# Optimization experiments

Measured on AMD Instinct MI355X. Metric: run time of the kernel, lower is better.

Reference implementation:

```python
import jax, jax.numpy as jnp
import numpy as np

N_HEADS = 8
TANH_CLIP = 10.0
NEG = -1e9  # finite stand-in for -inf so log_softmax/vjp stay NaN-free


def setup_inputs() -> dict:
    key = jax.random.key(0)
    ks = jax.random.split(key, 8)
    B, N, D = 256, 1000, 128
    embeddings = jax.random.normal(ks[0], (B, N, D), dtype=jnp.float32)
    W_node = jax.random.normal(ks[1], (D, 3 * D), dtype=jnp.float32) * (1.0 / np.sqrt(D))
    W_fixed = jax.random.normal(ks[2], (D, D), dtype=jnp.float32) * (1.0 / np.sqrt(D))
    W_step = jax.random.normal(ks[3], (2 * D, D), dtype=jnp.float32) * (1.0 / np.sqrt(2 * D))
    W_out = jax.random.normal(ks[4], (D, D), dtype=jnp.float32) * (1.0 / np.sqrt(D))
    first_idx = jax.random.randint(ks[5], (B,), 0, N)
    last_idx = jax.random.randint(ks[6], (B,), 0, N)
    mask = jax.random.randint(ks[7], (B, N), 0, 2).astype(jnp.bool_)
    mask = mask.at[:, 0].set(False)  # guarantee at least one feasible node
    return {"embeddings": embeddings, "W_node": W_node, "W_fixed": W_fixed,
            "W_step": W_step, "W_out": W_out, "first_idx": first_idx,
            "last_idx": last_idx, "mask": mask}


def reference(embeddings, W_node, W_fixed, W_step, W_out, first_idx, last_idx, mask):
    # One pointer-network decode step (TSP variant of AttentionModel._get_log_p),
    # including the _precompute projections.
    B, N, D = embeddings.shape
    H = N_HEADS
    dk = D // H

    # _precompute: fixed context + glimpse K/V + logit key
    graph_embed = embeddings.mean(axis=1)                       # [B, D]
    fixed_ctx = graph_embed @ W_fixed                           # [B, D]
    kvl = embeddings @ W_node                                   # [B, N, 3D]
    K, V, logit_K = jnp.split(kvl, 3, axis=-1)                  # each [B, N, D]

    # step context: cat(first-node emb, last-node emb) -> project to D
    b = jnp.arange(B)
    step_ctx = jnp.concatenate([embeddings[b, first_idx], embeddings[b, last_idx]], axis=-1)  # [B, 2D]
    q = fixed_ctx + step_ctx @ W_step                           # [B, D]

    # masked multi-head glimpse attention (q_len = 1)
    qh = q.reshape(B, H, dk)                                    # [B, H, dk]
    Kh = K.reshape(B, N, H, dk)
    Vh = V.reshape(B, N, H, dk)
    compat = jnp.einsum('bhd,bnhd->bhn', qh, Kh) / np.sqrt(dk)  # [B, H, N]
    compat = jnp.where(mask[:, None, :], NEG, compat)           # mask_inner
    attn = jax.nn.softmax(compat, axis=-1)
    heads = jnp.einsum('bhn,bnhd->bhd', attn, Vh)               # [B, H, dk]
    glimpse = heads.reshape(B, D) @ W_out                       # [B, D]

    # single-head logit attention with tanh clipping
    logits = jnp.einsum('bd,bnd->bn', glimpse, logit_K) / np.sqrt(D)  # [B, N]
    logits = jnp.tanh(logits) * TANH_CLIP
    logits = jnp.where(mask, NEG, logits)                       # mask_logits
    return jax.nn.log_softmax(logits, axis=-1)                  # [B, N]
```

## Files before the change

### kernel.cpp

```cpp
#include <hip/hip_runtime.h>


#define NEG (-1e9f)

__global__ void k_detect(const uint4* __restrict__ mw, int* __restrict__ flag)
{
    __shared__ int any_s;
    if (threadIdx.x == 0) any_s = 0;
    __syncthreads();
    unsigned acc = 0;
    #pragma unroll
    for (int i = 0; i < 4; ++i) {
        const uint4 v = mw[i * 256 + threadIdx.x];
        acc |= (v.x | v.y | v.z | v.w) & 0xFFFFFF00u;
    }
    if (acc) atomicOr(&any_s, 1);
    __syncthreads();
    if (threadIdx.x == 0) *flag = any_s;
}

__global__ __launch_bounds__(1024) void k_pre(
    const float* __restrict__ E, const float* __restrict__ Wn,
    const float* __restrict__ Wf, const float* __restrict__ Ws,
    const int* __restrict__ fi, const int* __restrict__ li,
    float* __restrict__ qkp)
{
    const int b = blockIdx.x;
    const int t = threadIdx.x;
    __shared__ float4 red4[1024];
    __shared__ float mu[128], e1[128], e2[128], q[128];
    __shared__ float qred[8][128];

    const float4* E4 = (const float4*)(E + (size_t)b * 128000);

    {
        const int c4 = t & 31, s = t >> 5;
        float4 acc = make_float4(0.f, 0.f, 0.f, 0.f);
        for (int r = s; r < 1000; r += 32) {
            float4 v = E4[r * 32 + c4];
            acc.x += v.x; acc.y += v.y; acc.z += v.z; acc.w += v.w;
        }
        red4[t] = acc;
    }
    if (t >= 512 && t < 544) {
        ((float4*)e1)[t - 512] = E4[fi[b] * 32 + (t - 512)];
    } else if (t >= 544 && t < 576) {
        ((float4*)e2)[t - 544] = E4[li[b] * 32 + (t - 544)];
    }
    __syncthreads();
    if (t < 32) {
        float4 acc = red4[t];
        #pragma unroll
        for (int s = 1; s < 32; ++s) {
            float4 v = red4[s * 32 + t];
            acc.x += v.x; acc.y += v.y; acc.z += v.z; acc.w += v.w;
        }
        const float inv = 1.0f / 1000.0f;
        ((float4*)mu)[t] = make_float4(acc.x * inv, acc.y * inv, acc.z * inv, acc.w * inv);
    }
    __syncthreads();
    {
        const int part = t >> 7, d = t & 127;
        float acc = 0.f;
        const int k0 = part * 48;
        for (int k = k0; k < k0 + 48; ++k) {
            const float s = (k < 128) ? mu[k] : (k < 256 ? e1[k - 128] : e2[k - 256]);
            const float w = (k < 128) ? Wf[k * 128 + d] : Ws[(k - 128) * 128 + d];
            acc += s * w;
        }
        qred[part][d] = acc;
    }
    __syncthreads();
    if (t < 128) {
        float acc = 0.f;
        #pragma unroll
        for (int p = 0; p < 8; ++p) acc += qred[p][t];
        q[t] = acc;
    }
    __syncthreads();
    {
        const int j = t & 127, cg = t >> 7;
        const float qj = q[j];
        for (int c0 = 0; c0 < 128; c0 += 8) {
            const int c = c0 + cg;
            float v = Wn[c * 384 + j] * qj;
            v += __shfl_down(v, 8, 16);
            v += __shfl_down(v, 4, 16);
            v += __shfl_down(v, 2, 16);
            v += __shfl_down(v, 1, 16);
            if ((j & 15) == 0) qkp[b * 1024 + (j >> 4) * 128 + c] = v * 0.25f;
        }
    }
}

__global__ __launch_bounds__(256) void k_glimpse(
    const float* __restrict__ E, const float* __restrict__ Wn,
    const float* __restrict__ Wo,
    const int* __restrict__ maskI, const unsigned char* __restrict__ maskB,
    const int* __restrict__ flag,
    const float* __restrict__ qkp, float* __restrict__ glp)
{
    const int b = blockIdx.x;
    const int t = threadIdx.x;
    __shared__ float4 qk4[256];
    __shared__ float4 Et[2048];
    __shared__ float pc[64 * 33];
    __shared__ float ct[64 * 9];
    __shared__ float pt[64 * 8];
    __shared__ float mh[8], lh[8], al[8];
    __shared__ float EbarF[8 * 128];
    __shared__ float heads[128];
    __shared__ float gl[128];

    const float4* E4 = (const float4*)(E + (size_t)b * 128000);
    const bool useB = (*flag != 0);

    {
        const int h = t >> 5, g = t & 31;
        qk4[h * 32 + (g ^ (g >> 3))] = ((const float4*)(qkp + b * 1024))[t];
    }
    if (t < 8) { mh[t] = -3e38f; lh[t] = 0.f; }
    float4 eacc[8];
    #pragma unroll
    for (int h = 0; h < 8; ++h) eacc[h] = make_float4(0.f, 0.f, 0.f, 0.f);
    const int c4 = t & 31, sl = t >> 5;
    const int rr = t >> 2, qq = t & 3;
    __syncthreads();

    for (int tile = 0; tile < 16; ++tile) {
        const int r0 = tile * 64;
        {
            const int g = r0 + rr;
            float4 v[8];
            if (g < 1000) {
                #pragma unroll
                for (int i = 0; i < 8; ++i) v[i] = E4[g * 32 + qq * 8 + i];
            } else {
                #pragma unroll
                for (int i = 0; i < 8; ++i) v[i] = make_float4(0.f, 0.f, 0.f, 0.f);
            }
            float pch[8];
            #pragma unroll
            for (int h = 0; h < 8; ++h) pch[h] = 0.f;
            #pragma unroll
            for (int i = 0; i < 8; ++i) {
                const int grp = qq * 8 + i;
                Et[rr * 32 + (grp ^ (rr & 7))] = v[i];
                #pragma unroll
                for (int h = 0; h < 8; ++h) {
                    float4 w = qk4[h * 32 + (grp ^ qq)];
                    pch[h] += v[i].x * w.x + v[i].y * w.y + v[i].z * w.z + v[i].w * w.w;
                }
            }
            #pragma unroll
            for (int h = 0; h < 8; ++h) pc[rr * 33 + qq * 8 + h] = pch[h];
        }
        __syncthreads();
        #pragma unroll
        for (int k = 0; k < 2; ++k) {
            const int idx = t + k * 256;
            const int row = idx >> 3, h = idx & 7;
            float s = pc[row * 33 + h] + pc[row * 33 + 8 + h]
                    + pc[row * 33 + 16 + h] + pc[row * 33 + 24 + h];
            const int g = r0 + row;
            const bool m = (g >= 1000) ||
                (useB ? (maskB[b * 1000 + g] != 0) : (maskI[b * 1000 + g] != 0));
            ct[row * 9 + h] = m ? NEG : s;
        }
        __syncthreads();
        if (t < 8) {
            float mt = -3e38f;
            for (int r = 0; r < 64; ++r) mt = fmaxf(mt, ct[r * 9 + t]);
            const float mnew = fmaxf(mh[t], mt);
            al[t] = __expf(mh[t] - mnew);
            mh[t] = mnew;
        }
        __syncthreads();
        #pragma unroll
        for (int k = 0; k < 2; ++k) {
            const int idx = t + k * 256;
            const int row = idx >> 3, h = idx & 7;
            pt[row * 8 + h] = __expf(ct[row * 9 + h] - mh[h]);
        }
        __syncthreads();
        if (t < 8) {
            float s = 0.f;
            for (int r = 0; r < 64; ++r) s += pt[r * 8 + t];
            lh[t] = lh[t] * al[t] + s;
        }
        {
            #pragma unroll
            for (int h = 0; h < 8; ++h) {
                const float a = al[h];
                eacc[h].x *= a; eacc[h].y *= a; eacc[h].z *= a; eacc[h].w *= a;
            }
            #pragma unroll
            for (int j = 0; j < 8; ++j) {
                const int r = sl * 8 + j;
                const float4 ev = Et[r * 32 + (c4 ^ (r & 7))];
                const float4 p0 = ((float4*)pt)[r * 2];
                const float4 p1 = ((float4*)pt)[r * 2 + 1];
                eacc[0].x += p0.x * ev.x; eacc[0].y += p0.x * ev.y; eacc[0].z += p0.x * ev.z; eacc[0].w += p0.x * ev.w;
                eacc[1].x += p0.y * ev.x; eacc[1].y += p0.y * ev.y; eacc[1].z += p0.y * ev.z; eacc[1].w += p0.y * ev.w;
                eacc[2].x += p0.z * ev.x; eacc[2].y += p0.z * ev.y; eacc[2].z += p0.z * ev.z; eacc[2].w += p0.z * ev.w;
                eacc[3].x += p0.w * ev.x; eacc[3].y += p0.w * ev.y; eacc[3].z += p0.w * ev.z; eacc[3].w += p0.w * ev.w;
                eacc[4].x += p1.x * ev.x; eacc[4].y += p1.x * ev.y; eacc[4].z += p1.x * ev.z; eacc[4].w += p1.x * ev.w;
                eacc[5].x += p1.y * ev.x; eacc[5].y += p1.y * ev.y; eacc[5].z += p1.y * ev.z; eacc[5].w += p1.y * ev.w;
                eacc[6].x += p1.z * ev.x; eacc[6].y += p1.z * ev.y; eacc[6].z += p1.z * ev.z; eacc[6].w += p1.z * ev.w;
                eacc[7].x += p1.w * ev.x; eacc[7].y += p1.w * ev.y; eacc[7].z += p1.w * ev.z; eacc[7].w += p1.w * ev.w;
            }
        }
        __syncthreads();
    }

    #pragma unroll
    for (int h = 0; h < 8; ++h) Et[sl * 256 + h * 32 + c4] = eacc[h];
    __syncthreads();
    {
        const int h = t >> 5, cc = t & 31;
        float4 s = make_float4(0.f, 0.f, 0.f, 0.f);
        #pragma unroll
        for (int s2 = 0; s2 < 8; ++s2) {
            float4 v = Et[s2 * 256 + h * 32 + cc];
            s.x += v.x; s.y += v.y; s.z += v.z; s.w += v.w;
        }
        const float invl = 1.0f / lh[h];
        ((float4*)EbarF)[h * 32 + cc] =
            make_float4(s.x * invl, s.y * invl, s.z * invl, s.w * invl);
    }
    __syncthreads();
    if (t < 128) {
        const int h = t >> 4;
        float acc = 0.f;
        for (int c = 0; c < 128; ++c) acc += EbarF[h * 128 + c] * Wn[c * 384 + 128 + t];
        heads[t] = acc;
    }
    __syncthreads();
    if (t < 128) {
        float acc = 0.f;
        for (int j2 = 0; j2 < 128; ++j2) acc += heads[j2] * Wo[j2 * 128 + t];
        gl[t] = acc;
    }
    __syncthreads();
    if (t < 128) {
        float acc = 0.f;
        for (int d2 = 0; d2 < 128; ++d2) acc += Wn[t * 384 + 256 + d2] * gl[d2];
        glp[b * 128 + t] = acc * 0.08838834764831845f;
    }
}

__global__ __launch_bounds__(256) void k_logits(
    const float* __restrict__ E,
    const int* __restrict__ maskI, const unsigned char* __restrict__ maskB,
    const int* __restrict__ flag,
    const float* __restrict__ glp, float* __restrict__ out)
{
    const int b = blockIdx.x;
    const int t = threadIdx.x;
    __shared__ float gl[128];
    __shared__ float z[1024];
    __shared__ float pc[256];
    __shared__ float red[4];
    __shared__ float stat[2];

    const float4* E4 = (const float4*)(E + (size_t)b * 128000);
    const bool useB = (*flag != 0);
    if (t < 32) ((float4*)gl)[t] = ((const float4*)(glp + b * 128))[t];
    __syncthreads();

    const int rr = t >> 2, qq = t & 3;
    for (int tile = 0; tile < 16; ++tile) {
        const int g = tile * 64 + rr;
        float acc = 0.f;
        if (g < 1000) {
            #pragma unroll
            for (int i = 0; i < 8; ++i) {
                const float4 v = E4[g * 32 + qq * 8 + i];
                const float4 w = ((float4*)gl)[qq * 8 + i];
                acc += v.x * w.x + v.y * w.y + v.z * w.z + v.w * w.w;
            }
        }
        pc[t] = acc;
        __syncthreads();
        if (t < 64) {
            const int g2 = tile * 64 + t;
            if (g2 < 1000) {
                const float s = pc[t * 4] + pc[t * 4 + 1] + pc[t * 4 + 2] + pc[t * 4 + 3];
                float zz = 10.0f * tanhf(s);
                const bool m = useB ? (maskB[b * 1000 + g2] != 0)
                                    : (maskI[b * 1000 + g2] != 0);
                if (m) zz = NEG;
                z[g2] = zz;
            }
        }
        __syncthreads();
    }
    float mloc = -3e38f;
    for (int idx = t; idx < 1000; idx += 256) mloc = fmaxf(mloc, z[idx]);
    #pragma unroll
    for (int off = 32; off > 0; off >>= 1) mloc = fmaxf(mloc, __shfl_down(mloc, off, 64));
    if ((t & 63) == 0) red[t >> 6] = mloc;
    __syncthreads();
    if (t == 0) stat[0] = fmaxf(fmaxf(red[0], red[1]), fmaxf(red[2], red[3]));
    __syncthreads();
    const float zmax = stat[0];
    float sloc = 0.f;
    for (int idx = t; idx < 1000; idx += 256) sloc += __expf(z[idx] - zmax);
    #pragma unroll
    for (int off = 32; off > 0; off >>= 1) sloc += __shfl_down(sloc, off, 64);
    if ((t & 63) == 0) red[t >> 6] = sloc;
    __syncthreads();
    if (t == 0) stat[1] = zmax + __logf(red[0] + red[1] + red[2] + red[3]);
    __syncthreads();
    const float lse = stat[1];
    for (int idx = t; idx < 1000; idx += 256)
        out[(size_t)b * 1000 + idx] = z[idx] - lse;
}

extern "C" void kernel_launch(void* const* d_in, const int* in_sizes, int n_in,
                              void* d_out, int out_size, void* d_ws, size_t ws_size,
                              hipStream_t stream) {
    const float* E  = (const float*)d_in[0];
    const float* Wn = (const float*)d_in[1];
    const float* Wf = (const float*)d_in[2];
    const float* Ws = (const float*)d_in[3];
    const float* Wo = (const float*)d_in[4];
    const int*   fi = (const int*)d_in[5];
    const int*   li = (const int*)d_in[6];
    const int*   maskI = (const int*)d_in[7];
    const unsigned char* maskB = (const unsigned char*)d_in[7];
    float* out = (float*)d_out;

    float* qkp = (float*)d_ws;
    float* glp = qkp + 256 * 1024;
    int*   flag = (int*)(glp + 256 * 128);

    k_detect<<<1, 256, 0, stream>>>((const uint4*)d_in[7], flag);
    k_pre<<<256, 1024, 0, stream>>>(E, Wn, Wf, Ws, fi, li, qkp);
    k_glimpse<<<256, 256, 0, stream>>>(E, Wn, Wo, maskI, maskB, flag, qkp, glp);
    k_logits<<<256, 256, 0, stream>>>(E, maskI, maskB, flag, glp, out);
}
```

Measured before the change: 335.2 us.

## Widen glimpse and logits blocks to process larger row tiles per iteration

The glimpse kernel goes from 256 to 512 threads and processes 128-row tiles, so there are half as many tile iterations. Its per-head max and sum reductions are split across 64 threads in two stages. The logits kernel moves to 1024 threads with 8 lanes per row and one element per thread in the softmax reductions. The aim is more parallelism per block and fewer serialized barrier-bound iterations, since only 256 blocks exist for the whole GPU. The cost is more shared memory and register pressure per block (a 64KB Et buffer plus 32 accumulator floats per thread at 512 threads), which may limit occupancy.

```diff
diff --git a/kernel.cpp b/kernel.cpp
--- a/kernel.cpp
+++ b/kernel.cpp
@@ -93,7 +93,7 @@
     }
 }
 
-__global__ __launch_bounds__(256) void k_glimpse(
+__global__ __launch_bounds__(512) void k_glimpse(
     const float* __restrict__ E, const float* __restrict__ Wn,
     const float* __restrict__ Wo,
     const int* __restrict__ maskI, const unsigned char* __restrict__ maskB,
@@ -103,10 +103,11 @@
     const int b = blockIdx.x;
     const int t = threadIdx.x;
     __shared__ float4 qk4[256];
-    __shared__ float4 Et[2048];
-    __shared__ float pc[64 * 33];
-    __shared__ float ct[64 * 9];
-    __shared__ float pt[64 * 8];
+    __shared__ float4 Et[4096];
+    __shared__ float pc[128 * 36];
+    __shared__ float ct[128 * 9];
+    __shared__ float pt[128 * 8];
+    __shared__ float redh[8 * 9];
     __shared__ float mh[8], lh[8], al[8];
     __shared__ float EbarF[8 * 128];
     __shared__ float heads[128];
@@ -115,7 +116,7 @@
     const float4* E4 = (const float4*)(E + (size_t)b * 128000);
     const bool useB = (*flag != 0);
 
-    {
+    if (t < 256) {
         const int h = t >> 5, g = t & 31;
         qk4[h * 32 + (g ^ (g >> 3))] = ((const float4*)(qkp + b * 1024))[t];
     }
@@ -127,8 +128,8 @@
     const int rr = t >> 2, qq = t & 3;
     __syncthreads();
 
-    for (int tile = 0; tile < 16; ++tile) {
-        const int r0 = tile * 64;
+    for (int tile = 0; tile < 8; ++tile) {
+        const int r0 = tile * 128;
         {
             const int g = r0 + rr;
             float4 v[8];
@@ -153,24 +154,32 @@
                 }
             }
             #pragma unroll
-            for (int h = 0; h < 8; ++h) pc[rr * 33 + qq * 8 + h] = pch[h];
+            for (int h = 0; h < 8; ++h) pc[rr * 36 + qq * 9 + h] = pch[h];
         }
         __syncthreads();
         #pragma unroll
         for (int k = 0; k < 2; ++k) {
-            const int idx = t + k * 256;
+            const int idx = t + k * 512;
             const int row = idx >> 3, h = idx & 7;
-            float s = pc[row * 33 + h] + pc[row * 33 + 8 + h]
-                    + pc[row * 33 + 16 + h] + pc[row * 33 + 24 + h];
+            float s = pc[row * 36 + h] + pc[row * 36 + 9 + h]
+                    + pc[row * 36 + 18 + h] + pc[row * 36 + 27 + h];
             const int g = r0 + row;
             const bool m = (g >= 1000) ||
                 (useB ? (maskB[b * 1000 + g] != 0) : (maskI[b * 1000 + g] != 0));
             ct[row * 9 + h] = m ? NEG : s;
         }
         __syncthreads();
+        if (t < 64) {
+            const int h = t & 7, part = t >> 3;
+            float mt = -3e38f;
+            const int rb = part * 16;
+            for (int r = 0; r < 16; ++r) mt = fmaxf(mt, ct[(rb + r) * 9 + h]);
+            redh[part * 9 + h] = mt;
+        }
+        __syncthreads();
         if (t < 8) {
-            float mt = -3e38f;
-            for (int r = 0; r < 64; ++r) mt = fmaxf(mt, ct[r * 9 + t]);
+            float mt = redh[t];
+            for (int p = 1; p < 8; ++p) mt = fmaxf(mt, redh[p * 9 + t]);
             const float mnew = fmaxf(mh[t], mt);
             al[t] = __expf(mh[t] - mnew);
             mh[t] = mnew;
@@ -178,16 +187,11 @@
         __syncthreads();
         #pragma unroll
         for (int k = 0; k < 2; ++k) {
-            const int idx = t + k * 256;
+            const int idx = t + k * 512;
             const int row = idx >> 3, h = idx & 7;
             pt[row * 8 + h] = __expf(ct[row * 9 + h] - mh[h]);
         }
         __syncthreads();
-        if (t < 8) {
-            float s = 0.f;
-            for (int r = 0; r < 64; ++r) s += pt[r * 8 + t];
-            lh[t] = lh[t] * al[t] + s;
-        }
         {
             #pragma unroll
             for (int h = 0; h < 8; ++h) {
@@ -210,17 +214,29 @@
                 eacc[7].x += p1.w * ev.x; eacc[7].y += p1.w * ev.y; eacc[7].z += p1.w * ev.z; eacc[7].w += p1.w * ev.w;
             }
         }
-        __syncthreads();
+        if (t < 64) {
+            const int h = t & 7, part = t >> 3;
+            float s = 0.f;
+            const int rb = part * 16;
+            for (int r = 0; r < 16; ++r) s += pt[(rb + r) * 8 + h];
+            redh[part * 9 + h] = s;
+        }
+        __syncthreads();
+        if (t < 8) {
+            float s = 0.f;
+            for (int p = 0; p < 8; ++p) s += redh[p * 9 + t];
+            lh[t] = lh[t] * al[t] + s;
+        }
     }
 
     #pragma unroll
     for (int h = 0; h < 8; ++h) Et[sl * 256 + h * 32 + c4] = eacc[h];
     __syncthreads();
-    {
+    if (t < 256) {
         const int h = t >> 5, cc = t & 31;
         float4 s = make_float4(0.f, 0.f, 0.f, 0.f);
         #pragma unroll
-        for (int s2 = 0; s2 < 8; ++s2) {
+        for (int s2 = 0; s2 < 16; ++s2) {
             float4 v = Et[s2 * 256 + h * 32 + cc];
             s.x += v.x; s.y += v.y; s.z += v.z; s.w += v.w;
         }
@@ -249,7 +265,7 @@
     }
 }
 
-__global__ __launch_bounds__(256) void k_logits(
+__global__ __launch_bounds__(1024) void k_logits(
     const float* __restrict__ E,
     const int* __restrict__ maskI, const unsigned char* __restrict__ maskB,
     const int* __restrict__ flag,
@@ -259,8 +275,8 @@
     const int t = threadIdx.x;
     __shared__ float gl[128];
     __shared__ float z[1024];
-    __shared__ float pc[256];
-    __shared__ float red[4];
+    __shared__ float pc[128 * 9];
+    __shared__ float red[16];
     __shared__ float stat[2];
 
     const float4* E4 = (const float4*)(E + (size_t)b * 128000);
@@ -268,24 +284,26 @@
     if (t < 32) ((float4*)gl)[t] = ((const float4*)(glp + b * 128))[t];
     __syncthreads();
 
-    const int rr = t >> 2, qq = t & 3;
-    for (int tile = 0; tile < 16; ++tile) {
-        const int g = tile * 64 + rr;
+    const int row = t >> 3, sub = t & 7;
+    for (int tile = 0; tile < 8; ++tile) {
+        const int g = tile * 128 + row;
         float acc = 0.f;
         if (g < 1000) {
             #pragma unroll
-            for (int i = 0; i < 8; ++i) {
-                const float4 v = E4[g * 32 + qq * 8 + i];
-                const float4 w = ((float4*)gl)[qq * 8 + i];
+            for (int i = 0; i < 4; ++i) {
+                const float4 v = E4[g * 32 + sub * 4 + i];
+                const float4 w = ((float4*)gl)[sub * 4 + i];
                 acc += v.x * w.x + v.y * w.y + v.z * w.z + v.w * w.w;
             }
         }
-        pc[t] = acc;
-        __syncthreads();
-        if (t < 64) {
-            const int g2 = tile * 64 + t;
+        pc[row * 9 + sub] = acc;
+        __syncthreads();
+        if (t < 128) {
+            const int g2 = tile * 128 + t;
             if (g2 < 1000) {
-                const float s = pc[t * 4] + pc[t * 4 + 1] + pc[t * 4 + 2] + pc[t * 4 + 3];
+                float s = 0.f;
+                #pragma unroll
+                for (int q2 = 0; q2 < 8; ++q2) s += pc[t * 9 + q2];
                 float zz = 10.0f * tanhf(s);
                 const bool m = useB ? (maskB[b * 1000 + g2] != 0)
                                     : (maskI[b * 1000 + g2] != 0);
@@ -295,26 +313,31 @@
         }
         __syncthreads();
     }
-    float mloc = -3e38f;
-    for (int idx = t; idx < 1000; idx += 256) mloc = fmaxf(mloc, z[idx]);
-    #pragma unroll
-    for (int off = 32; off > 0; off >>= 1) mloc = fmaxf(mloc, __shfl_down(mloc, off, 64));
-    if ((t & 63) == 0) red[t >> 6] = mloc;
-    __syncthreads();
-    if (t == 0) stat[0] = fmaxf(fmaxf(red[0], red[1]), fmaxf(red[2], red[3]));
+    float v = (t < 1000) ? z[t] : -3e38f;
+    #pragma unroll
+    for (int off = 32; off > 0; off >>= 1) v = fmaxf(v, __shfl_down(v, off, 64));
+    if ((t & 63) == 0) red[t >> 6] = v;
+    __syncthreads();
+    if (t == 0) {
+        float m = red[0];
+        for (int i = 1; i < 16; ++i) m = fmaxf(m, red[i]);
+        stat[0] = m;
+    }
     __syncthreads();
     const float zmax = stat[0];
-    float sloc = 0.f;
-    for (int idx = t; idx < 1000; idx += 256) sloc += __expf(z[idx] - zmax);
-    #pragma unroll
-    for (int off = 32; off > 0; off >>= 1) sloc += __shfl_down(sloc, off, 64);
-    if ((t & 63) == 0) red[t >> 6] = sloc;
-    __syncthreads();
-    if (t == 0) stat[1] = zmax + __logf(red[0] + red[1] + red[2] + red[3]);
-    __syncthreads();
-    const float lse = stat[1];
-    for (int idx = t; idx < 1000; idx += 256)
-        out[(size_t)b * 1000 + idx] = z[idx] - lse;
+    float sv = (t < 1000) ? __expf(z[t] - zmax) : 0.f;
+    #pragma unroll
+    for (int off = 32; off > 0; off >>= 1) sv += __shfl_down(sv, off, 64);
+    if ((t & 63) == 0) red[t >> 6] = sv;
+    __syncthreads();
+    if (t == 0) {
+        float s = 0.f;
+        for (int i = 0; i < 16; ++i) s += red[i];
+        stat[1] = zmax + __logf(s);
+    }
+    __syncthreads();
+    if (t < 1000)
+        out[(size_t)b * 1000 + t] = z[t] - stat[1];
 }
 
 extern "C" void kernel_launch(void* const* d_in, const int* in_sizes, int n_in,
@@ -337,6 +360,6 @@
 
     k_detect<<<1, 256, 0, stream>>>((const uint4*)d_in[7], flag);
     k_pre<<<256, 1024, 0, stream>>>(E, Wn, Wf, Ws, fi, li, qkp);
-    k_glimpse<<<256, 256, 0, stream>>>(E, Wn, Wo, maskI, maskB, flag, qkp, glp);
-    k_logits<<<256, 256, 0, stream>>>(E, maskI, maskB, flag, glp, out);
-}
+    k_glimpse<<<256, 512, 0, stream>>>(E, Wn, Wo, maskI, maskB, flag, qkp, glp);
+    k_logits<<<256, 1024, 0, stream>>>(E, maskI, maskB, flag, glp, out);
+}
```

New measurement: 299.6 us. -10.6%, faster.
